# Kernel optimization log

Hardware: AMD Instinct MI355X
Metric: run time of the kernel (lower is better)

The kernel has to match this reference:

```python
import jax, jax.numpy as jnp
import numpy as np

N_HEAD = 16

def setup_inputs() -> dict:
    key = jax.random.key(0)
    ks = jax.random.split(key, 5)
    B, T, C = 2, 2048, 1024
    s = 1.0 / np.sqrt(C)
    return {
        "x": jax.random.normal(ks[0], (B, T, C), dtype=jnp.float32),
        "Wq": jax.random.normal(ks[1], (C, C), dtype=jnp.float32) * s,
        "Wk": jax.random.normal(ks[2], (C, C), dtype=jnp.float32) * s,
        "Wv": jax.random.normal(ks[3], (C, C), dtype=jnp.float32) * s,
        "Wo": jax.random.normal(ks[4], (C, C), dtype=jnp.float32) * s,
        "bo": jnp.zeros((C,), dtype=jnp.float32),
    }

def reference(x, Wq, Wk, Wv, Wo, bo):
    B, T, C = x.shape
    H = N_HEAD
    D = C // H

    def shape(t):  # (B,T,C) -> (B,H,T,D)
        return t.reshape(B, T, H, D).transpose(0, 2, 1, 3)

    q = shape(x @ Wq)
    k = shape(x @ Wk)
    v = shape(x @ Wv)

    # scores: (B,H,T,Tk), Tk == T (no past_kv)
    att = jnp.einsum("bhtd,bhsd->bhts", q, k) * (1.0 / np.sqrt(D))
    i = jnp.arange(T)[:, None]
    j = jnp.arange(T)[None, :]
    causal = (j <= i)  # (T, Tk)
    att = jnp.where(causal[None, None], att, -jnp.inf)
    att = jax.nn.softmax(att, axis=-1)  # dropout=0.0 -> identity

    out = jnp.einsum("bhts,bhsd->bhtd", att, v)
    out = out.transpose(0, 2, 1, 3).reshape(B, T, C)
    out = out @ Wo + bo
    return out, (k, v)
```

## Files before the change

kernel.cpp:

```cpp
#include <hip/hip_runtime.h>
#include <hip/hip_bf16.h>

constexpr int B_ = 2;
constexpr int T_ = 2048;
constexpr int C_ = 1024;
constexpr int H_ = 16;
constexpr int D_ = 64;
constexpr int M_ = B_ * T_;

typedef __attribute__((ext_vector_type(8))) short bf16x8;
typedef __attribute__((ext_vector_type(4))) float f32x4;
typedef const __attribute__((address_space(1))) void gaddr_t;
typedef __attribute__((address_space(3))) void laddr_t;

__device__ __forceinline__ unsigned short f2bf(float f) {
    unsigned u = __float_as_uint(f);
    return (unsigned short)((u + 0x7fffu + ((u >> 16) & 1u)) >> 16);
}

union BF8 { bf16x8 v; __hip_bfloat162 h[4]; };

__device__ __forceinline__ bf16x8 cvt8(const float4 a, const float4 b) {
    BF8 r;
    r.h[0] = __float22bfloat162_rn(make_float2(a.x, a.y));
    r.h[1] = __float22bfloat162_rn(make_float2(a.z, a.w));
    r.h[2] = __float22bfloat162_rn(make_float2(b.x, b.y));
    r.h[3] = __float22bfloat162_rn(make_float2(b.z, b.w));
    return r.v;
}

__global__ __launch_bounds__(256)
void prep(const float* __restrict__ x, const float* __restrict__ Wq,
          const float* __restrict__ Wk, const float* __restrict__ Wv,
          const float* __restrict__ Wo, unsigned short* __restrict__ xb,
          unsigned short* __restrict__ wtb)
{
    const int z = blockIdx.z;
    const int tid = threadIdx.x;

    if (z == 4) {
        const int base = (blockIdx.y * 16 + blockIdx.x) * 4096 + tid;
#pragma unroll
        for (int i = 0; i < 16; ++i) {
            const int idx = base + i * 256;
            float4 v = ((const float4*)x)[idx];
            union { __hip_bfloat162 h[2]; ushort4 u; } o;
            o.h[0] = __float22bfloat162_rn(make_float2(v.x, v.y));
            o.h[1] = __float22bfloat162_rn(make_float2(v.z, v.w));
            ((ushort4*)xb)[idx] = o.u;
        }
        return;
    }

    __shared__ float tile[64][65];
    const float* W = (z == 0) ? Wq : (z == 1) ? Wk : (z == 2) ? Wv : Wo;
    unsigned short* O = wtb + (size_t)z * C_ * C_;

    const int n0 = blockIdx.x * 64, k0 = blockIdx.y * 64;
    const int r = tid >> 4, c4 = (tid & 15) * 4;

#pragma unroll
    for (int i = 0; i < 4; ++i) {
        const int kk = i * 16 + r;
        float4 v = *(const float4*)(W + (size_t)(k0 + kk) * C_ + n0 + c4);
        tile[c4 + 0][kk] = v.x;
        tile[c4 + 1][kk] = v.y;
        tile[c4 + 2][kk] = v.z;
        tile[c4 + 3][kk] = v.w;
    }
    __syncthreads();
#pragma unroll
    for (int i = 0; i < 4; ++i) {
        const int nn = i * 16 + r;
        ushort4 o;
        o.x = f2bf(tile[nn][c4 + 0]);
        o.y = f2bf(tile[nn][c4 + 1]);
        o.z = f2bf(tile[nn][c4 + 2]);
        o.w = f2bf(tile[nn][c4 + 3]);
        *(ushort4*)(O + (size_t)(n0 + nn) * C_ + k0 + c4) = o;
    }
}

template<int WRITE_KB>
__global__ __launch_bounds__(256)
void gemm_qkv(const unsigned short* __restrict__ xb, const unsigned short* __restrict__ wtb,
              unsigned short* __restrict__ qb, float* __restrict__ kout,
              float* __restrict__ vout, unsigned short* __restrict__ kb,
              unsigned short* __restrict__ vtt)
{
    __shared__ unsigned short As[128 * 64];
    __shared__ unsigned short Bs[128 * 64];

    const int tid = threadIdx.x;

    const int flat = blockIdx.y * 24 + blockIdx.x;
    const int l = (flat & 7) * 96 + (flat >> 3);
    const int m0 = (l / 24) * 128;
    const int xc = l % 24;
    const int which = xc >> 3;
    const int n0 = (xc & 7) * 128;
    const unsigned short* wt = wtb + (size_t)which * C_ * C_;

    const int lane = tid & 63, w = tid >> 6;
    const int wm = (w >> 1) * 64, wn = (w & 1) * 64;
    const int fr = lane & 15, qd = lane >> 4;

    f32x4 acc[4][4] = {};

    for (int k0 = 0; k0 < C_; k0 += 64) {
#pragma unroll
        for (int cc = 0; cc < 4; ++cc) {
            const int c = tid + cc * 256;
            const int row = c >> 3, dg = (c & 7) ^ (row & 7);
            __builtin_amdgcn_global_load_lds(
                (gaddr_t*)(xb + (size_t)(m0 + row) * C_ + k0 + dg * 8),
                (laddr_t*)((char*)As + (size_t)c * 16), 16, 0, 0);
        }
#pragma unroll
        for (int cc = 0; cc < 4; ++cc) {
            const int c = tid + cc * 256;
            const int row = c >> 3, dg = (c & 7) ^ (row & 7);
            __builtin_amdgcn_global_load_lds(
                (gaddr_t*)(wt + (size_t)(n0 + row) * C_ + k0 + dg * 8),
                (laddr_t*)((char*)Bs + (size_t)c * 16), 16, 0, 0);
        }
        __syncthreads();

#pragma unroll
        for (int half = 0; half < 2; ++half) {
            bf16x8 af[4], bfv[4];
#pragma unroll
            for (int mt = 0; mt < 4; ++mt) {
                const int row = wm + mt * 16 + fr, dg = half * 4 + qd;
                af[mt] = *(const bf16x8*)&As[row * 64 + ((dg ^ (row & 7)) * 8)];
            }
#pragma unroll
            for (int nt = 0; nt < 4; ++nt) {
                const int row = wn + nt * 16 + fr, dg = half * 4 + qd;
                bfv[nt] = *(const bf16x8*)&Bs[row * 64 + ((dg ^ (row & 7)) * 8)];
            }
#pragma unroll
            for (int mt = 0; mt < 4; ++mt)
#pragma unroll
                for (int nt = 0; nt < 4; ++nt)
                    acc[mt][nt] = __builtin_amdgcn_mfma_f32_16x16x32_bf16(
                        bfv[nt], af[mt], acc[mt][nt], 0, 0, 0);
        }
        __syncthreads();
    }

#pragma unroll
    for (int mt = 0; mt < 4; ++mt) {
        const int mm = m0 + wm + mt * 16 + fr;
        const int b = mm >> 11, t = mm & (T_ - 1);
#pragma unroll
        for (int nt = 0; nt < 4; ++nt) {
            const int nn = n0 + wn + nt * 16 + qd * 4;
            const int h = nn >> 6, d0 = nn & 63;
            const int bh = b * H_ + h;
            const size_t off = ((size_t)bh * T_ + t) * D_ + d0;
            const f32x4 a4 = acc[mt][nt];
            if (which == 0) {
                *(ushort4*)(qb + off) =
                    make_ushort4(f2bf(a4[0]), f2bf(a4[1]), f2bf(a4[2]), f2bf(a4[3]));
            } else if (which == 1) {
                *(float4*)(kout + off) = make_float4(a4[0], a4[1], a4[2], a4[3]);
                if (WRITE_KB)
                    *(ushort4*)(kb + off) =
                        make_ushort4(f2bf(a4[0]), f2bf(a4[1]), f2bf(a4[2]), f2bf(a4[3]));
            } else {
                *(float4*)(vout + off) = make_float4(a4[0], a4[1], a4[2], a4[3]);
                unsigned short* vb = vtt
                    + (((size_t)bh * (T_ / 64) + (t >> 6)) * 64 + d0) * 64 + (t & 63);
#pragma unroll
                for (int r = 0; r < 4; ++r) vb[(size_t)r * 64] = f2bf(a4[r]);
            }
        }
    }
}

__global__ __launch_bounds__(256)
void gemm_o(const unsigned short* __restrict__ ab, const unsigned short* __restrict__ wot,
            const float* __restrict__ bo, float* __restrict__ out)
{
    __shared__ unsigned short As[128 * 64];
    __shared__ unsigned short Bs[64 * 64];

    const int tid = threadIdx.x;

    const int flat = blockIdx.y * 16 + blockIdx.x;
    const int l = (flat & 7) * 64 + (flat >> 3);
    const int m0 = (l / 16) * 128;
    const int n0 = (l % 16) * 64;

    const int lane = tid & 63, w = tid >> 6;
    const int wm = (w >> 1) * 64, wn = (w & 1) * 32;
    const int fr = lane & 15, qd = lane >> 4;

    f32x4 acc[4][2] = {};

    for (int k0 = 0; k0 < C_; k0 += 64) {
#pragma unroll
        for (int cc = 0; cc < 4; ++cc) {
            const int c = tid + cc * 256;
            const int row = c >> 3, dg = (c & 7) ^ (row & 7);
            __builtin_amdgcn_global_load_lds(
                (gaddr_t*)(ab + (size_t)(m0 + row) * C_ + k0 + dg * 8),
                (laddr_t*)((char*)As + (size_t)c * 16), 16, 0, 0);
        }
#pragma unroll
        for (int cc = 0; cc < 2; ++cc) {
            const int c = tid + cc * 256;
            const int row = c >> 3, dg = (c & 7) ^ (row & 7);
            __builtin_amdgcn_global_load_lds(
                (gaddr_t*)(wot + (size_t)(n0 + row) * C_ + k0 + dg * 8),
                (laddr_t*)((char*)Bs + (size_t)c * 16), 16, 0, 0);
        }
        __syncthreads();

#pragma unroll
        for (int half = 0; half < 2; ++half) {
            bf16x8 af[4], bfv[2];
#pragma unroll
            for (int mt = 0; mt < 4; ++mt) {
                const int row = wm + mt * 16 + fr, dg = half * 4 + qd;
                af[mt] = *(const bf16x8*)&As[row * 64 + ((dg ^ (row & 7)) * 8)];
            }
#pragma unroll
            for (int nt = 0; nt < 2; ++nt) {
                const int row = wn + nt * 16 + fr, dg = half * 4 + qd;
                bfv[nt] = *(const bf16x8*)&Bs[row * 64 + ((dg ^ (row & 7)) * 8)];
            }
#pragma unroll
            for (int mt = 0; mt < 4; ++mt)
#pragma unroll
                for (int nt = 0; nt < 2; ++nt)
                    acc[mt][nt] = __builtin_amdgcn_mfma_f32_16x16x32_bf16(
                        bfv[nt], af[mt], acc[mt][nt], 0, 0, 0);
        }
        __syncthreads();
    }

#pragma unroll
    for (int mt = 0; mt < 4; ++mt) {
        const int mm = m0 + wm + mt * 16 + fr;
#pragma unroll
        for (int nt = 0; nt < 2; ++nt) {
            const int nn = n0 + wn + nt * 16 + qd * 4;
            const float4 b4 = *(const float4*)(bo + nn);
            *(float4*)(out + (size_t)mm * C_ + nn) =
                make_float4(acc[mt][nt][0] + b4.x, acc[mt][nt][1] + b4.y,
                            acc[mt][nt][2] + b4.z, acc[mt][nt][3] + b4.w);
        }
    }
}

__global__ __launch_bounds__(256)
void attn_lds(const unsigned short* __restrict__ qb, const unsigned short* __restrict__ kb,
              const unsigned short* __restrict__ vtt, unsigned short* __restrict__ attb)
{
    __shared__ unsigned short Ks[2][64 * 64];
    __shared__ unsigned short Vs[2][64 * 64];
    __shared__ alignas(16) unsigned short Pt[4][16 * 72];

    const int tid = threadIdx.x;
    const int lane = tid & 63, w = tid >> 6;
    const int fr = lane & 15, qd = lane >> 4;

    const int blk = blockIdx.x;
    const int xcd = blk & 7, within = blk >> 3;
    const int bh = xcd * 4 + (within & 3);
    const int jj = within >> 2;
    const int kk_ = jj >> 3, ii_ = jj & 7;
    const int qt = (kk_ == 0) ? (31 - ii_) : (kk_ == 1) ? ii_
                 : (kk_ == 2) ? (23 - ii_) : (8 + ii_);
    const int b = bh >> 4, h = bh & 15;

    unsigned short* Pw = Pt[w];
    const unsigned short* qB = qb  + (size_t)bh * T_ * D_;
    const unsigned short* kB = kb  + (size_t)bh * T_ * D_;
    const unsigned short* vT = vtt + (size_t)bh * (T_ / 64) * 64 * 64;

    const int qr0 = qt * 64 + w * 16;
    const int qrow_g = qr0 + fr;

    bf16x8 aq0 = *(const bf16x8*)(qB + (size_t)(qr0 + fr) * D_ + qd * 8);
    bf16x8 aq1 = *(const bf16x8*)(qB + (size_t)(qr0 + fr) * D_ + 32 + qd * 8);

    f32x4 accT[4] = {};
    float l_i = 0.0f;
    const float sc2 = 0.18033688f;

    const int L0 = w * 128 + lane, L1 = L0 + 64;
    const int r0 = L0 >> 3, e0 = (((L0 & 7) ^ (r0 & 7)) * 8);
    const int r1 = L1 >> 3, e1 = (((L1 & 7) ^ (r1 & 7)) * 8);

    {
        __builtin_amdgcn_global_load_lds((gaddr_t*)(kB + r0 * 64 + e0),
            (laddr_t*)((char*)Ks[0] + (size_t)L0 * 16), 16, 0, 0);
        __builtin_amdgcn_global_load_lds((gaddr_t*)(kB + r1 * 64 + e1),
            (laddr_t*)((char*)Ks[0] + (size_t)L1 * 16), 16, 0, 0);
        __builtin_amdgcn_global_load_lds((gaddr_t*)(vT + r0 * 64 + e0),
            (laddr_t*)((char*)Vs[0] + (size_t)L0 * 16), 16, 0, 0);
        __builtin_amdgcn_global_load_lds((gaddr_t*)(vT + r1 * 64 + e1),
            (laddr_t*)((char*)Vs[0] + (size_t)L1 * 16), 16, 0, 0);
    }
    asm volatile("s_waitcnt vmcnt(0)" ::: "memory");
    __builtin_amdgcn_s_barrier();
    __builtin_amdgcn_sched_barrier(0);

    for (int jt = 0; jt <= qt; ++jt) {
        const int cur = jt & 1;
        if (jt < qt) {
            const unsigned short* kt = kB + (size_t)((jt + 1) * 64) * 64;
            const unsigned short* vt = vT + (size_t)(jt + 1) * 4096;
            char* Kn = (char*)Ks[cur ^ 1];
            char* Vn = (char*)Vs[cur ^ 1];
            __builtin_amdgcn_global_load_lds((gaddr_t*)(kt + r0 * 64 + e0),
                (laddr_t*)(Kn + (size_t)L0 * 16), 16, 0, 0);
            __builtin_amdgcn_global_load_lds((gaddr_t*)(kt + r1 * 64 + e1),
                (laddr_t*)(Kn + (size_t)L1 * 16), 16, 0, 0);
            __builtin_amdgcn_global_load_lds((gaddr_t*)(vt + r0 * 64 + e0),
                (laddr_t*)(Vn + (size_t)L0 * 16), 16, 0, 0);
            __builtin_amdgcn_global_load_lds((gaddr_t*)(vt + r1 * 64 + e1),
                (laddr_t*)(Vn + (size_t)L1 * 16), 16, 0, 0);
        }
        const unsigned short* Kc = Ks[cur];
        const unsigned short* Vc = Vs[cur];

        bf16x8 bk[8];
#pragma unroll
        for (int q8 = 0; q8 < 8; ++q8) {
            const int row = (q8 >> 1) * 16 + fr;
            const int dg = (q8 & 1) * 4 + qd;
            bk[q8] = *(const bf16x8*)&Kc[row * 64 + ((dg ^ (row & 7)) * 8)];
        }

        f32x4 s4[4] = {};
        __builtin_amdgcn_s_setprio(1);
#pragma unroll
        for (int nt = 0; nt < 4; ++nt) {
            s4[nt] = __builtin_amdgcn_mfma_f32_16x16x32_bf16(bk[nt * 2 + 0], aq0, s4[nt], 0, 0, 0);
            s4[nt] = __builtin_amdgcn_mfma_f32_16x16x32_bf16(bk[nt * 2 + 1], aq1, s4[nt], 0, 0, 0);
        }
        __builtin_amdgcn_s_setprio(0);

        if (jt == qt) {
            const int kbase = jt * 64 + qd * 4;
#pragma unroll
            for (int nt = 0; nt < 4; ++nt)
#pragma unroll
            for (int r = 0; r < 4; ++r) {
                const int kcol = kbase + nt * 16 + r;
                const float pv = (kcol <= qrow_g)
                               ? __builtin_amdgcn_exp2f(s4[nt][r] * sc2) : 0.0f;
                s4[nt][r] = pv;
                l_i += pv;
            }
        } else {
#pragma unroll
            for (int nt = 0; nt < 4; ++nt)
#pragma unroll
            for (int r = 0; r < 4; ++r) {
                const float pv = __builtin_amdgcn_exp2f(s4[nt][r] * sc2);
                s4[nt][r] = pv;
                l_i += pv;
            }
        }

#pragma unroll
        for (int nt = 0; nt < 4; ++nt) {
            union { __hip_bfloat162 h2[2]; unsigned long long u; } pk;
            pk.h2[0] = __float22bfloat162_rn(make_float2(s4[nt][0], s4[nt][1]));
            pk.h2[1] = __float22bfloat162_rn(make_float2(s4[nt][2], s4[nt][3]));
            *(unsigned long long*)&Pw[fr * 72 + nt * 16 + qd * 4] = pk.u;
        }
        const bf16x8 ap0 = *(const bf16x8*)&Pw[fr * 72 + qd * 8];
        const bf16x8 ap1 = *(const bf16x8*)&Pw[fr * 72 + 32 + qd * 8];

        bf16x8 bv[8];
#pragma unroll
        for (int q8 = 0; q8 < 8; ++q8) {
            const int row = (q8 >> 1) * 16 + fr;
            const int dg = (q8 & 1) * 4 + qd;
            bv[q8] = *(const bf16x8*)&Vc[row * 64 + ((dg ^ (row & 7)) * 8)];
        }

        __builtin_amdgcn_s_setprio(1);
#pragma unroll
        for (int nt = 0; nt < 4; ++nt) {
            accT[nt] = __builtin_amdgcn_mfma_f32_16x16x32_bf16(bv[nt * 2 + 0], ap0, accT[nt], 0, 0, 0);
            accT[nt] = __builtin_amdgcn_mfma_f32_16x16x32_bf16(bv[nt * 2 + 1], ap1, accT[nt], 0, 0, 0);
        }
        __builtin_amdgcn_s_setprio(0);

        asm volatile("s_waitcnt vmcnt(0)" ::: "memory");
        __builtin_amdgcn_s_barrier();
        __builtin_amdgcn_sched_barrier(0);
    }

    l_i += __shfl_xor(l_i, 16);
    l_i += __shfl_xor(l_i, 32);
    const float inv = 1.0f / l_i;

#pragma unroll
    for (int nt = 0; nt < 4; ++nt) {
        union { __hip_bfloat162 h2[2]; unsigned long long u; } ok;
        ok.h2[0] = __float22bfloat162_rn(make_float2(accT[nt][0] * inv, accT[nt][1] * inv));
        ok.h2[1] = __float22bfloat162_rn(make_float2(accT[nt][2] * inv, accT[nt][3] * inv));
        *(unsigned long long*)&Pw[fr * 72 + nt * 16 + qd * 4] = ok.u;
    }
    {
        const int row = lane >> 2, d0 = (lane & 3) * 16;
        const bf16x8 o0 = *(const bf16x8*)&Pw[row * 72 + d0];
        const bf16x8 o1 = *(const bf16x8*)&Pw[row * 72 + d0 + 8];
        unsigned short* op = attb + ((size_t)b * T_ + qr0 + row) * C_ + h * 64 + d0;
        *(bf16x8*)op = o0;
        *(bf16x8*)(op + 8) = o1;
    }
}

__global__ __launch_bounds__(256)
void attn_v4(const unsigned short* __restrict__ qb, const float* __restrict__ kf,
             const unsigned short* __restrict__ vtt, unsigned short* __restrict__ attb)
{
    __shared__ alignas(16) unsigned short Pt[4][16 * 72];

    const int tid = threadIdx.x;
    const int lane = tid & 63, w = tid >> 6;
    const int fr = lane & 15, qd = lane >> 4;

    const int blk = blockIdx.x;
    const int xcd = blk & 7, within = blk >> 3;
    const int bh = xcd * 4 + (within & 3);
    const int jj = within >> 2;
    const int kk_ = jj >> 3, ii_ = jj & 7;
    const int qt = (kk_ == 0) ? (31 - ii_) : (kk_ == 1) ? ii_
                 : (kk_ == 2) ? (23 - ii_) : (8 + ii_);
    const int b = bh >> 4, h = bh & 15;

    unsigned short* Pw = Pt[w];
    const unsigned short* qB = qb  + (size_t)bh * T_ * D_;
    const float*          kB = kf  + (size_t)bh * T_ * D_;
    const unsigned short* vT = vtt + (size_t)bh * (T_ / 64) * 64 * 64;

    const int qr0 = qt * 64 + w * 16;
    const int qrow_g = qr0 + fr;

    bf16x8 aq0 = *(const bf16x8*)(qB + (size_t)(qr0 + fr) * D_ + qd * 8);
    bf16x8 aq1 = *(const bf16x8*)(qB + (size_t)(qr0 + fr) * D_ + 32 + qd * 8);

    f32x4 accT[4] = {};
    float l_i = 0.0f;
    const float sc2 = 0.18033688f;

    for (int jt = 0; jt <= qt; ++jt) {
        bf16x8 bk[8];
#pragma unroll
        for (int q8 = 0; q8 < 8; ++q8) {
            const float* p = kB + (size_t)(jt * 64 + (q8 >> 1) * 16 + fr) * D_
                           + (q8 & 1) * 32 + qd * 8;
            bk[q8] = cvt8(*(const float4*)p, *(const float4*)(p + 4));
        }
        f32x4 s4[4] = {};
#pragma unroll
        for (int nt = 0; nt < 4; ++nt) {
            s4[nt] = __builtin_amdgcn_mfma_f32_16x16x32_bf16(bk[nt * 2 + 0], aq0, s4[nt], 0, 0, 0);
            s4[nt] = __builtin_amdgcn_mfma_f32_16x16x32_bf16(bk[nt * 2 + 1], aq1, s4[nt], 0, 0, 0);
        }
        if (jt == qt) {
            const int kbase = jt * 64 + qd * 4;
#pragma unroll
            for (int nt = 0; nt < 4; ++nt)
#pragma unroll
            for (int r = 0; r < 4; ++r) {
                const int kcol = kbase + nt * 16 + r;
                const float pv = (kcol <= qrow_g)
                               ? __builtin_amdgcn_exp2f(s4[nt][r] * sc2) : 0.0f;
                s4[nt][r] = pv; l_i += pv;
            }
        } else {
#pragma unroll
            for (int nt = 0; nt < 4; ++nt)
#pragma unroll
            for (int r = 0; r < 4; ++r) {
                const float pv = __builtin_amdgcn_exp2f(s4[nt][r] * sc2);
                s4[nt][r] = pv; l_i += pv;
            }
        }
#pragma unroll
        for (int nt = 0; nt < 4; ++nt) {
            union { __hip_bfloat162 h2[2]; unsigned long long u; } pk;
            pk.h2[0] = __float22bfloat162_rn(make_float2(s4[nt][0], s4[nt][1]));
            pk.h2[1] = __float22bfloat162_rn(make_float2(s4[nt][2], s4[nt][3]));
            *(unsigned long long*)&Pw[fr * 72 + nt * 16 + qd * 4] = pk.u;
        }
        const bf16x8 ap0 = *(const bf16x8*)&Pw[fr * 72 + qd * 8];
        const bf16x8 ap1 = *(const bf16x8*)&Pw[fr * 72 + 32 + qd * 8];

        bf16x8 bv[8];
#pragma unroll
        for (int q8 = 0; q8 < 8; ++q8)
            bv[q8] = *(const bf16x8*)(vT + (size_t)jt * 4096
                                      + ((q8 >> 1) * 16 + fr) * 64 + (q8 & 1) * 32 + qd * 8);
#pragma unroll
        for (int nt = 0; nt < 4; ++nt) {
            accT[nt] = __builtin_amdgcn_mfma_f32_16x16x32_bf16(bv[nt * 2 + 0], ap0, accT[nt], 0, 0, 0);
            accT[nt] = __builtin_amdgcn_mfma_f32_16x16x32_bf16(bv[nt * 2 + 1], ap1, accT[nt], 0, 0, 0);
        }
    }

    l_i += __shfl_xor(l_i, 16);
    l_i += __shfl_xor(l_i, 32);
    const float inv = 1.0f / l_i;
#pragma unroll
    for (int nt = 0; nt < 4; ++nt) {
        union { __hip_bfloat162 h2[2]; unsigned long long u; } ok;
        ok.h2[0] = __float22bfloat162_rn(make_float2(accT[nt][0] * inv, accT[nt][1] * inv));
        ok.h2[1] = __float22bfloat162_rn(make_float2(accT[nt][2] * inv, accT[nt][3] * inv));
        *(unsigned long long*)&Pw[fr * 72 + nt * 16 + qd * 4] = ok.u;
    }
    {
        const int row = lane >> 2, d0 = (lane & 3) * 16;
        const bf16x8 o0 = *(const bf16x8*)&Pw[row * 72 + d0];
        const bf16x8 o1 = *(const bf16x8*)&Pw[row * 72 + d0 + 8];
        unsigned short* op = attb + ((size_t)b * T_ + qr0 + row) * C_ + h * 64 + d0;
        *(bf16x8*)op = o0;
        *(bf16x8*)(op + 8) = o1;
    }
}

extern "C" void kernel_launch(void* const* d_in, const int* in_sizes, int n_in,
                              void* d_out, int out_size, void* d_ws, size_t ws_size,
                              hipStream_t stream)
{
    (void)in_sizes; (void)n_in; (void)out_size;
    const float* x  = (const float*)d_in[0];
    const float* Wq = (const float*)d_in[1];
    const float* Wk = (const float*)d_in[2];
    const float* Wv = (const float*)d_in[3];
    const float* Wo = (const float*)d_in[4];
    const float* bo = (const float*)d_in[5];

    float* out  = (float*)d_out;
    float* kout = out  + (size_t)M_ * C_;
    float* vout = kout + (size_t)B_ * H_ * T_ * D_;

    unsigned short* xb   = (unsigned short*)d_ws;
    unsigned short* wtb  = xb  + (size_t)M_ * C_;
    unsigned short* qb   = wtb + (size_t)4 * C_ * C_;
    unsigned short* vtt  = qb  + (size_t)M_ * C_;
    unsigned short* kb   = vtt + (size_t)M_ * C_;
    unsigned short* attb = xb;
    const bool use_kb = ws_size >= (size_t)40 * 1024 * 1024;

    prep<<<dim3(16, 16, 5), 256, 0, stream>>>(x, Wq, Wk, Wv, Wo, xb, wtb);

    if (use_kb)
        gemm_qkv<1><<<dim3(24, 32), 256, 0, stream>>>(xb, wtb, qb, kout, vout, kb, vtt);
    else
        gemm_qkv<0><<<dim3(24, 32), 256, 0, stream>>>(xb, wtb, qb, kout, vout, kb, vtt);

    if (use_kb)
        attn_lds<<<1024, 256, 0, stream>>>(qb, kb, vtt, attb);
    else
        attn_v4<<<1024, 256, 0, stream>>>(qb, kout, vtt, attb);

    gemm_o<<<dim3(16, 32), 256, 0, stream>>>(attb, wtb + (size_t)3 * C_ * C_, bo, out);
}
```

Baseline: 191.6 us.

## Use 128-row query tiles with 8 waves in attention; drop QKV GEMM block swizzle

```diff
diff --git a/kernel.cpp b/kernel.cpp
--- a/kernel.cpp
+++ b/kernel.cpp
@@ -92,13 +92,9 @@
     __shared__ unsigned short Bs[128 * 64];
 
     const int tid = threadIdx.x;
-
-    const int flat = blockIdx.y * 24 + blockIdx.x;
-    const int l = (flat & 7) * 96 + (flat >> 3);
-    const int m0 = (l / 24) * 128;
-    const int xc = l % 24;
-    const int which = xc >> 3;
-    const int n0 = (xc & 7) * 128;
+    const int which = blockIdx.x >> 3;
+    const int n0 = (blockIdx.x & 7) * 128;
+    const int m0 = blockIdx.y * 128;
     const unsigned short* wt = wtb + (size_t)which * C_ * C_;
 
     const int lane = tid & 63, w = tid >> 6;
@@ -255,13 +251,13 @@
     }
 }
 
-__global__ __launch_bounds__(256)
+__global__ __launch_bounds__(512)
 void attn_lds(const unsigned short* __restrict__ qb, const unsigned short* __restrict__ kb,
               const unsigned short* __restrict__ vtt, unsigned short* __restrict__ attb)
 {
     __shared__ unsigned short Ks[2][64 * 64];
     __shared__ unsigned short Vs[2][64 * 64];
-    __shared__ alignas(16) unsigned short Pt[4][16 * 72];
+    __shared__ alignas(16) unsigned short Pt[8][16 * 72];
 
     const int tid = threadIdx.x;
     const int lane = tid & 63, w = tid >> 6;
@@ -271,9 +267,7 @@
     const int xcd = blk & 7, within = blk >> 3;
     const int bh = xcd * 4 + (within & 3);
     const int jj = within >> 2;
-    const int kk_ = jj >> 3, ii_ = jj & 7;
-    const int qt = (kk_ == 0) ? (31 - ii_) : (kk_ == 1) ? ii_
-                 : (kk_ == 2) ? (23 - ii_) : (8 + ii_);
+    const int qt = (jj >> 3) == 0 ? (15 - (jj & 7)) : (jj & 7);
     const int b = bh >> 4, h = bh & 15;
 
     unsigned short* Pw = Pt[w];
@@ -281,8 +275,10 @@
     const unsigned short* kB = kb  + (size_t)bh * T_ * D_;
     const unsigned short* vT = vtt + (size_t)bh * (T_ / 64) * 64 * 64;
 
-    const int qr0 = qt * 64 + w * 16;
+    const int qr0 = qt * 128 + w * 16;
     const int qrow_g = qr0 + fr;
+    const int jtmax = 2 * qt + 1;
+    const int jt_diag = qr0 >> 6;
 
     bf16x8 aq0 = *(const bf16x8*)(qB + (size_t)(qr0 + fr) * D_ + qd * 8);
     bf16x8 aq1 = *(const bf16x8*)(qB + (size_t)(qr0 + fr) * D_ + 32 + qd * 8);
@@ -291,39 +287,26 @@
     float l_i = 0.0f;
     const float sc2 = 0.18033688f;
 
-    const int L0 = w * 128 + lane, L1 = L0 + 64;
+    const int L0 = tid;
     const int r0 = L0 >> 3, e0 = (((L0 & 7) ^ (r0 & 7)) * 8);
-    const int r1 = L1 >> 3, e1 = (((L1 & 7) ^ (r1 & 7)) * 8);
-
-    {
-        __builtin_amdgcn_global_load_lds((gaddr_t*)(kB + r0 * 64 + e0),
-            (laddr_t*)((char*)Ks[0] + (size_t)L0 * 16), 16, 0, 0);
-        __builtin_amdgcn_global_load_lds((gaddr_t*)(kB + r1 * 64 + e1),
-            (laddr_t*)((char*)Ks[0] + (size_t)L1 * 16), 16, 0, 0);
-        __builtin_amdgcn_global_load_lds((gaddr_t*)(vT + r0 * 64 + e0),
-            (laddr_t*)((char*)Vs[0] + (size_t)L0 * 16), 16, 0, 0);
-        __builtin_amdgcn_global_load_lds((gaddr_t*)(vT + r1 * 64 + e1),
-            (laddr_t*)((char*)Vs[0] + (size_t)L1 * 16), 16, 0, 0);
-    }
+
+    __builtin_amdgcn_global_load_lds((gaddr_t*)(kB + r0 * 64 + e0),
+        (laddr_t*)((char*)Ks[0] + (size_t)L0 * 16), 16, 0, 0);
+    __builtin_amdgcn_global_load_lds((gaddr_t*)(vT + r0 * 64 + e0),
+        (laddr_t*)((char*)Vs[0] + (size_t)L0 * 16), 16, 0, 0);
     asm volatile("s_waitcnt vmcnt(0)" ::: "memory");
     __builtin_amdgcn_s_barrier();
     __builtin_amdgcn_sched_barrier(0);
 
-    for (int jt = 0; jt <= qt; ++jt) {
+    for (int jt = 0; jt <= jtmax; ++jt) {
         const int cur = jt & 1;
-        if (jt < qt) {
+        if (jt < jtmax) {
             const unsigned short* kt = kB + (size_t)((jt + 1) * 64) * 64;
             const unsigned short* vt = vT + (size_t)(jt + 1) * 4096;
-            char* Kn = (char*)Ks[cur ^ 1];
-            char* Vn = (char*)Vs[cur ^ 1];
             __builtin_amdgcn_global_load_lds((gaddr_t*)(kt + r0 * 64 + e0),
-                (laddr_t*)(Kn + (size_t)L0 * 16), 16, 0, 0);
-            __builtin_amdgcn_global_load_lds((gaddr_t*)(kt + r1 * 64 + e1),
-                (laddr_t*)(Kn + (size_t)L1 * 16), 16, 0, 0);
+                (laddr_t*)((char*)Ks[cur ^ 1] + (size_t)L0 * 16), 16, 0, 0);
             __builtin_amdgcn_global_load_lds((gaddr_t*)(vt + r0 * 64 + e0),
-                (laddr_t*)(Vn + (size_t)L0 * 16), 16, 0, 0);
-            __builtin_amdgcn_global_load_lds((gaddr_t*)(vt + r1 * 64 + e1),
-                (laddr_t*)(Vn + (size_t)L1 * 16), 16, 0, 0);
+                (laddr_t*)((char*)Vs[cur ^ 1] + (size_t)L0 * 16), 16, 0, 0);
         }
         const unsigned short* Kc = Ks[cur];
         const unsigned short* Vc = Vs[cur];
@@ -345,7 +328,7 @@
         }
         __builtin_amdgcn_s_setprio(0);
 
-        if (jt == qt) {
+        if (jt >= jt_diag) {
             const int kbase = jt * 64 + qd * 4;
 #pragma unroll
             for (int nt = 0; nt < 4; ++nt)
@@ -562,7 +545,7 @@
         gemm_qkv<0><<<dim3(24, 32), 256, 0, stream>>>(xb, wtb, qb, kout, vout, kb, vtt);
 
     if (use_kb)
-        attn_lds<<<1024, 256, 0, stream>>>(qb, kb, vtt, attb);
+        attn_lds<<<512, 512, 0, stream>>>(qb, kb, vtt, attb);
     else
         attn_v4<<<1024, 256, 0, stream>>>(qb, kout, vtt, attb);
 
```

Measured after the change: 194.2 us. Within noise of the previous version (+1.3%).

## Triple-buffer QKV and output GEMMs with 512-thread blocks and async prefetch

Applied to the files above, without the earlier changes.

```diff
diff --git a/kernel.cpp b/kernel.cpp
--- a/kernel.cpp
+++ b/kernel.cpp
@@ -82,80 +82,97 @@
 }
 
 template<int WRITE_KB>
-__global__ __launch_bounds__(256)
+__global__ __launch_bounds__(512)
 void gemm_qkv(const unsigned short* __restrict__ xb, const unsigned short* __restrict__ wtb,
               unsigned short* __restrict__ qb, float* __restrict__ kout,
               float* __restrict__ vout, unsigned short* __restrict__ kb,
               unsigned short* __restrict__ vtt)
 {
-    __shared__ unsigned short As[128 * 64];
-    __shared__ unsigned short Bs[128 * 64];
+    __shared__ unsigned short As[3][128 * 64];
+    __shared__ unsigned short Bs[3][128 * 64];
 
     const int tid = threadIdx.x;
-
-    const int flat = blockIdx.y * 24 + blockIdx.x;
-    const int l = (flat & 7) * 96 + (flat >> 3);
-    const int m0 = (l / 24) * 128;
-    const int xc = l % 24;
-    const int which = xc >> 3;
-    const int n0 = (xc & 7) * 128;
+    const int which = blockIdx.x >> 3;
+    const int n0 = (blockIdx.x & 7) * 128;
+    const int m0 = blockIdx.y * 128;
     const unsigned short* wt = wtb + (size_t)which * C_ * C_;
 
     const int lane = tid & 63, w = tid >> 6;
-    const int wm = (w >> 1) * 64, wn = (w & 1) * 64;
+    const int wm = (w >> 2) * 64, wn2 = (w & 3) * 32;
     const int fr = lane & 15, qd = lane >> 4;
 
-    f32x4 acc[4][4] = {};
-
-    for (int k0 = 0; k0 < C_; k0 += 64) {
-#pragma unroll
-        for (int cc = 0; cc < 4; ++cc) {
-            const int c = tid + cc * 256;
-            const int row = c >> 3, dg = (c & 7) ^ (row & 7);
-            __builtin_amdgcn_global_load_lds(
-                (gaddr_t*)(xb + (size_t)(m0 + row) * C_ + k0 + dg * 8),
-                (laddr_t*)((char*)As + (size_t)c * 16), 16, 0, 0);
-        }
-#pragma unroll
-        for (int cc = 0; cc < 4; ++cc) {
-            const int c = tid + cc * 256;
-            const int row = c >> 3, dg = (c & 7) ^ (row & 7);
-            __builtin_amdgcn_global_load_lds(
-                (gaddr_t*)(wt + (size_t)(n0 + row) * C_ + k0 + dg * 8),
-                (laddr_t*)((char*)Bs + (size_t)c * 16), 16, 0, 0);
-        }
-        __syncthreads();
-
+    int crow[2], cofs[2]; size_t clds[2];
+#pragma unroll
+    for (int cc = 0; cc < 2; ++cc) {
+        const int c = tid + cc * 512;
+        crow[cc] = c >> 3;
+        cofs[cc] = ((c & 7) ^ (crow[cc] & 7)) * 8;
+        clds[cc] = (size_t)c * 16;
+    }
+
+#define STAGE(s, kt)                                                               \
+    {                                                                              \
+        _Pragma("unroll")                                                          \
+        for (int cc = 0; cc < 2; ++cc) {                                           \
+            __builtin_amdgcn_global_load_lds(                                      \
+                (gaddr_t*)(xb + (size_t)(m0 + crow[cc]) * C_ + (kt) * 64 + cofs[cc]), \
+                (laddr_t*)((char*)As[s] + clds[cc]), 16, 0, 0);                    \
+            __builtin_amdgcn_global_load_lds(                                      \
+                (gaddr_t*)(wt + (size_t)(n0 + crow[cc]) * C_ + (kt) * 64 + cofs[cc]), \
+                (laddr_t*)((char*)Bs[s] + clds[cc]), 16, 0, 0);                    \
+        }                                                                          \
+    }
+
+    f32x4 acc[4][2] = {};
+    constexpr int NT = C_ / 64;
+
+    STAGE(0, 0);
+    STAGE(1, 1);
+    asm volatile("s_waitcnt vmcnt(4)" ::: "memory");
+    __builtin_amdgcn_s_barrier();
+    __builtin_amdgcn_sched_barrier(0);
+
+    for (int t = 0; t < NT; ++t) {
+        const int s = t % 3;
+        if (t + 2 < NT) STAGE((t + 2) % 3, t + 2);
+
+        const unsigned short* Ac = As[s];
+        const unsigned short* Bc = Bs[s];
 #pragma unroll
         for (int half = 0; half < 2; ++half) {
-            bf16x8 af[4], bfv[4];
+            bf16x8 af[4], bfv[2];
 #pragma unroll
             for (int mt = 0; mt < 4; ++mt) {
                 const int row = wm + mt * 16 + fr, dg = half * 4 + qd;
-                af[mt] = *(const bf16x8*)&As[row * 64 + ((dg ^ (row & 7)) * 8)];
-            }
-#pragma unroll
-            for (int nt = 0; nt < 4; ++nt) {
-                const int row = wn + nt * 16 + fr, dg = half * 4 + qd;
-                bfv[nt] = *(const bf16x8*)&Bs[row * 64 + ((dg ^ (row & 7)) * 8)];
+                af[mt] = *(const bf16x8*)&Ac[row * 64 + ((dg ^ (row & 7)) * 8)];
+            }
+#pragma unroll
+            for (int nt = 0; nt < 2; ++nt) {
+                const int row = wn2 + nt * 16 + fr, dg = half * 4 + qd;
+                bfv[nt] = *(const bf16x8*)&Bc[row * 64 + ((dg ^ (row & 7)) * 8)];
             }
 #pragma unroll
             for (int mt = 0; mt < 4; ++mt)
 #pragma unroll
-                for (int nt = 0; nt < 4; ++nt)
+                for (int nt = 0; nt < 2; ++nt)
                     acc[mt][nt] = __builtin_amdgcn_mfma_f32_16x16x32_bf16(
                         bfv[nt], af[mt], acc[mt][nt], 0, 0, 0);
         }
-        __syncthreads();
-    }
+
+        if (t + 2 < NT)      asm volatile("s_waitcnt vmcnt(4)" ::: "memory");
+        else if (t + 1 < NT) asm volatile("s_waitcnt vmcnt(0)" ::: "memory");
+        __builtin_amdgcn_s_barrier();
+        __builtin_amdgcn_sched_barrier(0);
+    }
+#undef STAGE
 
 #pragma unroll
     for (int mt = 0; mt < 4; ++mt) {
         const int mm = m0 + wm + mt * 16 + fr;
         const int b = mm >> 11, t = mm & (T_ - 1);
 #pragma unroll
-        for (int nt = 0; nt < 4; ++nt) {
-            const int nn = n0 + wn + nt * 16 + qd * 4;
+        for (int nt = 0; nt < 2; ++nt) {
+            const int nn = n0 + wn2 + nt * 16 + qd * 4;
             const int h = nn >> 6, d0 = nn & 63;
             const int bh = b * H_ + h;
             const size_t off = ((size_t)bh * T_ + t) * D_ + d0;
@@ -179,57 +196,70 @@
     }
 }
 
-__global__ __launch_bounds__(256)
+__global__ __launch_bounds__(512)
 void gemm_o(const unsigned short* __restrict__ ab, const unsigned short* __restrict__ wot,
             const float* __restrict__ bo, float* __restrict__ out)
 {
-    __shared__ unsigned short As[128 * 64];
-    __shared__ unsigned short Bs[64 * 64];
+    __shared__ unsigned short As[3][128 * 64];
+    __shared__ unsigned short Bs[3][128 * 64];
 
     const int tid = threadIdx.x;
-
-    const int flat = blockIdx.y * 16 + blockIdx.x;
-    const int l = (flat & 7) * 64 + (flat >> 3);
-    const int m0 = (l / 16) * 128;
-    const int n0 = (l % 16) * 64;
+    const int n0 = blockIdx.x * 128;
+    const int m0 = blockIdx.y * 128;
 
     const int lane = tid & 63, w = tid >> 6;
-    const int wm = (w >> 1) * 64, wn = (w & 1) * 32;
+    const int wm = (w >> 2) * 64, wn2 = (w & 3) * 32;
     const int fr = lane & 15, qd = lane >> 4;
 
+    int crow[2], cofs[2]; size_t clds[2];
+#pragma unroll
+    for (int cc = 0; cc < 2; ++cc) {
+        const int c = tid + cc * 512;
+        crow[cc] = c >> 3;
+        cofs[cc] = ((c & 7) ^ (crow[cc] & 7)) * 8;
+        clds[cc] = (size_t)c * 16;
+    }
+
+#define STAGE_O(s, kt)                                                             \
+    {                                                                              \
+        _Pragma("unroll")                                                          \
+        for (int cc = 0; cc < 2; ++cc) {                                           \
+            __builtin_amdgcn_global_load_lds(                                      \
+                (gaddr_t*)(ab + (size_t)(m0 + crow[cc]) * C_ + (kt) * 64 + cofs[cc]),  \
+                (laddr_t*)((char*)As[s] + clds[cc]), 16, 0, 0);                    \
+            __builtin_amdgcn_global_load_lds(                                      \
+                (gaddr_t*)(wot + (size_t)(n0 + crow[cc]) * C_ + (kt) * 64 + cofs[cc]), \
+                (laddr_t*)((char*)Bs[s] + clds[cc]), 16, 0, 0);                    \
+        }                                                                          \
+    }
+
     f32x4 acc[4][2] = {};
-
-    for (int k0 = 0; k0 < C_; k0 += 64) {
-#pragma unroll
-        for (int cc = 0; cc < 4; ++cc) {
-            const int c = tid + cc * 256;
-            const int row = c >> 3, dg = (c & 7) ^ (row & 7);
-            __builtin_amdgcn_global_load_lds(
-                (gaddr_t*)(ab + (size_t)(m0 + row) * C_ + k0 + dg * 8),
-                (laddr_t*)((char*)As + (size_t)c * 16), 16, 0, 0);
-        }
-#pragma unroll
-        for (int cc = 0; cc < 2; ++cc) {
-            const int c = tid + cc * 256;
-            const int row = c >> 3, dg = (c & 7) ^ (row & 7);
-            __builtin_amdgcn_global_load_lds(
-                (gaddr_t*)(wot + (size_t)(n0 + row) * C_ + k0 + dg * 8),
-                (laddr_t*)((char*)Bs + (size_t)c * 16), 16, 0, 0);
-        }
-        __syncthreads();
-
+    constexpr int NT = C_ / 64;
+
+    STAGE_O(0, 0);
+    STAGE_O(1, 1);
+    asm volatile("s_waitcnt vmcnt(4)" ::: "memory");
+    __builtin_amdgcn_s_barrier();
+    __builtin_amdgcn_sched_barrier(0);
+
+    for (int t = 0; t < NT; ++t) {
+        const int s = t % 3;
+        if (t + 2 < NT) STAGE_O((t + 2) % 3, t + 2);
+
+        const unsigned short* Ac = As[s];
+        const unsigned short* Bc = Bs[s];
 #pragma unroll
         for (int half = 0; half < 2; ++half) {
             bf16x8 af[4], bfv[2];
 #pragma unroll
             for (int mt = 0; mt < 4; ++mt) {
                 const int row = wm + mt * 16 + fr, dg = half * 4 + qd;
-                af[mt] = *(const bf16x8*)&As[row * 64 + ((dg ^ (row & 7)) * 8)];
+                af[mt] = *(const bf16x8*)&Ac[row * 64 + ((dg ^ (row & 7)) * 8)];
             }
 #pragma unroll
             for (int nt = 0; nt < 2; ++nt) {
-                const int row = wn + nt * 16 + fr, dg = half * 4 + qd;
-                bfv[nt] = *(const bf16x8*)&Bs[row * 64 + ((dg ^ (row & 7)) * 8)];
+                const int row = wn2 + nt * 16 + fr, dg = half * 4 + qd;
+                bfv[nt] = *(const bf16x8*)&Bc[row * 64 + ((dg ^ (row & 7)) * 8)];
             }
 #pragma unroll
             for (int mt = 0; mt < 4; ++mt)
@@ -238,15 +268,20 @@
                     acc[mt][nt] = __builtin_amdgcn_mfma_f32_16x16x32_bf16(
                         bfv[nt], af[mt], acc[mt][nt], 0, 0, 0);
         }
-        __syncthreads();
-    }
+
+        if (t + 2 < NT)      asm volatile("s_waitcnt vmcnt(4)" ::: "memory");
+        else if (t + 1 < NT) asm volatile("s_waitcnt vmcnt(0)" ::: "memory");
+        __builtin_amdgcn_s_barrier();
+        __builtin_amdgcn_sched_barrier(0);
+    }
+#undef STAGE_O
 
 #pragma unroll
     for (int mt = 0; mt < 4; ++mt) {
         const int mm = m0 + wm + mt * 16 + fr;
 #pragma unroll
         for (int nt = 0; nt < 2; ++nt) {
-            const int nn = n0 + wn + nt * 16 + qd * 4;
+            const int nn = n0 + wn2 + nt * 16 + qd * 4;
             const float4 b4 = *(const float4*)(bo + nn);
             *(float4*)(out + (size_t)mm * C_ + nn) =
                 make_float4(acc[mt][nt][0] + b4.x, acc[mt][nt][1] + b4.y,
@@ -557,14 +592,14 @@
     prep<<<dim3(16, 16, 5), 256, 0, stream>>>(x, Wq, Wk, Wv, Wo, xb, wtb);
 
     if (use_kb)
-        gemm_qkv<1><<<dim3(24, 32), 256, 0, stream>>>(xb, wtb, qb, kout, vout, kb, vtt);
+        gemm_qkv<1><<<dim3(24, 32), 512, 0, stream>>>(xb, wtb, qb, kout, vout, kb, vtt);
     else
-        gemm_qkv<0><<<dim3(24, 32), 256, 0, stream>>>(xb, wtb, qb, kout, vout, kb, vtt);
+        gemm_qkv<0><<<dim3(24, 32), 512, 0, stream>>>(xb, wtb, qb, kout, vout, kb, vtt);
 
     if (use_kb)
         attn_lds<<<1024, 256, 0, stream>>>(qb, kb, vtt, attb);
     else
         attn_v4<<<1024, 256, 0, stream>>>(qb, kout, vtt, attb);
 
-    gemm_o<<<dim3(16, 32), 256, 0, stream>>>(attb, wtb + (size_t)3 * C_ * C_, bo, out);
-}
+    gemm_o<<<dim3(8, 32), 512, 0, stream>>>(attb, wtb + (size_t)3 * C_ * C_, bo, out);
+}
```

Result: faster. 187.2 us (-2.3%).
